# Kernel tuning notes

Hardware: AMD Instinct MI355X
Metric: run time of the kernel (lower is better)

Reference implementation:

```python
import jax, jax.numpy as jnp
import numpy as np

D_MODEL = 768
N_HEADS = 8
HEAD_DIM = D_MODEL // N_HEADS
D_FF = 3072
EPS = 1e-5


def _layernorm(x, g, b):
    mu = jnp.mean(x, axis=-1, keepdims=True)
    var = jnp.var(x, axis=-1, keepdims=True)
    return (x - mu) * jax.lax.rsqrt(var + EPS) * g + b


def setup_inputs() -> dict:
    key = jax.random.key(0)
    ks = jax.random.split(key, 12)
    s = 0.02
    return {
        "x": jax.random.normal(ks[0], (2, 4096, D_MODEL), dtype=jnp.float32),
        "w_qkv": jax.random.normal(ks[1], (D_MODEL, 3 * D_MODEL), dtype=jnp.float32) * s,
        "b_qkv": jnp.zeros((3 * D_MODEL,), dtype=jnp.float32),
        "w_out": jax.random.normal(ks[2], (D_MODEL, D_MODEL), dtype=jnp.float32) * s,
        "b_out": jnp.zeros((D_MODEL,), dtype=jnp.float32),
        "w_ff1": jax.random.normal(ks[3], (D_MODEL, D_FF), dtype=jnp.float32) * s,
        "b_ff1": jnp.zeros((D_FF,), dtype=jnp.float32),
        "w_ff2": jax.random.normal(ks[4], (D_FF, D_MODEL), dtype=jnp.float32) * s,
        "b_ff2": jnp.zeros((D_MODEL,), dtype=jnp.float32),
        "g1": jnp.ones((D_MODEL,), dtype=jnp.float32),
        "be1": jnp.zeros((D_MODEL,), dtype=jnp.float32),
        "g2": jnp.ones((D_MODEL,), dtype=jnp.float32),
        "be2": jnp.zeros((D_MODEL,), dtype=jnp.float32),
    }


def reference(x, w_qkv, b_qkv, w_out, b_out, w_ff1, b_ff1, w_ff2, b_ff2, g1, be1, g2, be2):
    B, S, D = x.shape
    qkv = x @ w_qkv + b_qkv  # [B,S,3D]
    q, k, v = jnp.split(qkv, 3, axis=-1)
    # [B,H,S,d]
    q = q.reshape(B, S, N_HEADS, HEAD_DIM).transpose(0, 2, 1, 3)
    k = k.reshape(B, S, N_HEADS, HEAD_DIM).transpose(0, 2, 1, 3)
    v = v.reshape(B, S, N_HEADS, HEAD_DIM).transpose(0, 2, 1, 3)
    scores = jnp.einsum("bhqd,bhkd->bhqk", q, k) / np.sqrt(HEAD_DIM).astype(np.float32)
    attn = jax.nn.softmax(scores, axis=-1)
    out = jnp.einsum("bhqk,bhkd->bhqd", attn, v)
    out = out.transpose(0, 2, 1, 3).reshape(B, S, D)
    out = out @ w_out + b_out
    x = _layernorm(x + out, g1, be1)
    h = jax.nn.gelu(x @ w_ff1 + b_ff1, approximate=False)
    ffn = h @ w_ff2 + b_ff2
    return _layernorm(x + ffn, g2, be2)
```

## Files before the change

kernel.cpp:

```cpp
#include <hip/hip_runtime.h>
#include <hip/hip_bf16.h>
#include <stdint.h>


typedef __attribute__((ext_vector_type(8))) short bf16x8;
typedef __attribute__((ext_vector_type(4))) short bf16x4;
typedef __attribute__((ext_vector_type(4))) float f32x4;

#define MFMA_BF16(a, b, c) __builtin_amdgcn_mfma_f32_16x16x32_bf16((a), (b), (c), 0, 0, 0)

#define EXP2R(x) __builtin_amdgcn_exp2f(x)

__device__ __forceinline__ short f2bs(float f) {
  return __builtin_bit_cast(short, __float2bfloat16(f));
}
__device__ __forceinline__ float bs2f(short s) {
  union { unsigned u; float f; } v;
  v.u = ((unsigned)(unsigned short)s) << 16;
  return v.f;
}

__device__ __forceinline__ void gload16(const void* g, void* l) {
  __builtin_amdgcn_global_load_lds(
      (const __attribute__((address_space(1))) unsigned int*)g,
      (__attribute__((address_space(3))) unsigned int*)l, 16, 0, 0);
}

__device__ __forceinline__ unsigned ldsoff(const void* p) {
  return (unsigned)(uintptr_t)p;
}

#define TRD(dst, base, off) \
  asm volatile("ds_read_b64_tr_b16 %0, %1 offset:" #off : "=v"(dst) : "v"(base) : "memory")

__global__ __launch_bounds__(256) void transpose_cast(const float* __restrict__ W,
                                                      short* __restrict__ Wt,
                                                      int K, int N) {
  __shared__ float tile[32][33];
  const int n0 = blockIdx.x * 32, k0 = blockIdx.y * 32;
  const int tx = threadIdx.x & 31, ty = threadIdx.x >> 5;
#pragma unroll
  for (int i = 0; i < 4; ++i)
    tile[ty + i * 8][tx] = W[(size_t)(k0 + ty + i * 8) * N + n0 + tx];
  __syncthreads();
#pragma unroll
  for (int i = 0; i < 4; ++i)
    Wt[(size_t)(n0 + ty + i * 8) * K + k0 + tx] = f2bs(tile[tx][ty + i * 8]);
}

__global__ __launch_bounds__(256) void cast_bf16(const float* __restrict__ x,
                                                 short* __restrict__ y, int n4) {
  const int i = blockIdx.x * 256 + threadIdx.x;
  if (i < n4) {
    const float4 v = *(const float4*)(x + (size_t)i * 4);
    short4 o;
    o.x = f2bs(v.x); o.y = f2bs(v.y); o.z = f2bs(v.z); o.w = f2bs(v.w);
    *(short4*)(y + (size_t)i * 4) = o;
  }
}

template <int EPI>
__global__ __launch_bounds__(256) void gemm_bt(const short* __restrict__ A,
                                               const short* __restrict__ Bt,
                                               const float* __restrict__ bias,
                                               void* __restrict__ outp,
                                               int N, int K) {
  __shared__ __align__(16) short ls[3][10240];
  const int tid = threadIdx.x;
  const int lane = tid & 63, w = tid >> 6;
  const int lo = lane & 15, hi = lane >> 4;
  const int wr = w >> 1, wc = w & 1;

  const unsigned gdx = gridDim.x;
  const unsigned nwg = gdx * gridDim.y;
  unsigned lin = blockIdx.y * gdx + blockIdx.x;
  if ((nwg & 7u) == 0u) lin = (lin & 7u) * (nwg >> 3) + (lin >> 3);
  const unsigned by = lin / gdx, bx = lin - by * gdx;
  const int m0 = by * 128, n0 = bx * 128;

  f32x4 acc[4][4] = {};

  const short* rowsrc[5];
#pragma unroll
  for (int s = 0; s < 5; ++s) {
    const int u = s * 256 + tid;
    const int chunk = u / 320;
    const int uin = u - chunk * 320;
    const int r = uin / 5, ui = uin - r * 5;
    const int koff = (ui < 4) ? ui * 8 : 0;
    rowsrc[s] = (chunk < 2 ? A + (size_t)(m0 + chunk * 64 + r) * K
                           : Bt + (size_t)(n0 + (chunk - 2) * 64 + r) * K) + koff;
  }

  auto stage = [&](int kt, int buf) {
    char* base = (char*)ls[buf] + w * 1024;
#pragma unroll
    for (int s = 0; s < 5; ++s)
      gload16(rowsrc[s] + kt, base + s * 4096);
  };

  const int nk = K >> 5;
  stage(0, 0);
  stage(32, 1);
  int cur = 0, nxt = 2;
  for (int t = 0; t < nk; ++t) {
    if (t + 1 < nk) asm volatile("s_waitcnt vmcnt(5)" ::: "memory");
    else            asm volatile("s_waitcnt vmcnt(0)" ::: "memory");
    __builtin_amdgcn_s_barrier();
    asm volatile("" ::: "memory");
    if (t + 2 < nk) stage((t + 2) << 5, nxt);
    bf16x8 af[4], bfr[4];
    const char* lbase = (const char*)ls[cur];
#pragma unroll
    for (int i = 0; i < 4; ++i) {
      af[i]  = *(const bf16x8*)(lbase + (wr * 64 + i * 16 + lo) * 80 + hi * 16);
      bfr[i] = *(const bf16x8*)(lbase + 10240 + (wc * 64 + i * 16 + lo) * 80 + hi * 16);
    }
#pragma unroll
    for (int mi = 0; mi < 4; ++mi)
#pragma unroll
      for (int ni = 0; ni < 4; ++ni)
        acc[mi][ni] = MFMA_BF16(af[mi], bfr[ni], acc[mi][ni]);
    cur = cur == 2 ? 0 : cur + 1;
    nxt = nxt == 2 ? 0 : nxt + 1;
  }

  const int rb = m0 + wr * 64, cb = n0 + wc * 64;
#pragma unroll
  for (int ni = 0; ni < 4; ++ni) {
    const int col = cb + ni * 16 + lo;
    const float bc = bias[col];
#pragma unroll
    for (int mi = 0; mi < 4; ++mi) {
#pragma unroll
      for (int r = 0; r < 4; ++r) {
        const int row = rb + mi * 16 + hi * 4 + r;
        const float v = acc[mi][ni][r] + bc;
        if constexpr (EPI == 0) {
          const int which = col / 768, rem = col - which * 768;
          const int hh = rem / 96, d = rem - hh * 96;
          const int bb = row >> 12, ss = row & 4095;
          ((short*)outp)[((size_t)((which * 2 + bb) * 8 + hh) * 4096 + ss) * 96 + d] = f2bs(v);
        } else if constexpr (EPI == 1) {
          ((short*)outp)[(size_t)row * N + col] = f2bs(v);
        } else {
          const float ge = 0.5f * v * (1.f + erff(v * 0.70710678118654752f));
          ((short*)outp)[(size_t)row * N + col] = f2bs(ge);
        }
      }
    }
  }
}

__global__ __launch_bounds__(256, 3) void attn_fwd(const short* __restrict__ qkv,
                                                   short* __restrict__ out) {
  constexpr int SEQ = 4096;
  constexpr int NT = SEQ / 64;
  constexpr float SCALE2 = 0.10206207261596575f * 1.44269504088896f;
  constexpr float THR2 = 11.5415603f;
  const unsigned linear = blockIdx.x + 32u * (blockIdx.y + 8u * blockIdx.z);
  const int qt = linear >> 4;
  const int hb = linear & 15;
  const int h = hb & 7, b = hb >> 3;
  const int tid = threadIdx.x;
  const int lane = tid & 63, w = tid >> 6;
  const int lo = lane & 15, hi = lane >> 4;

  const size_t headsz = (size_t)SEQ * 96;
  const short* Qh = qkv + (size_t)((0 * 2 + b) * 8 + h) * headsz;
  const short* Kh = qkv + (size_t)((1 * 2 + b) * 8 + h) * headsz;
  const short* Vh = qkv + (size_t)((2 * 2 + b) * 8 + h) * headsz;

  __shared__ __align__(16) short k_lds[6144];
  __shared__ __align__(16) short v_lds[2][6144];
  __shared__ __align__(16) short p_lds[4][2048];

  int voff[3];
#pragma unroll
  for (int t = 0; t < 3; ++t) {
    const int c = t * 256 + tid;
    const int kq = c / 48, rem = c - kq * 48;
    const int dhi = rem >> 3, rem2 = rem & 7;
    voff[t] = (kq * 4 + (rem2 >> 1)) * 96 + dhi * 16 + (rem2 & 1) * 8;
  }

  const int qbase = qt * 128 + w * 32;
  bf16x8 qf[2][3];
#pragma unroll
  for (int f = 0; f < 2; ++f)
#pragma unroll
    for (int dk = 0; dk < 3; ++dk) {
      bf16x8 v = *(const bf16x8*)(Qh + (size_t)(qbase + f * 16 + lo) * 96 + dk * 32 + hi * 8);
#pragma unroll
      for (int i = 0; i < 8; ++i) v[i] = f2bs(bs2f(v[i]) * SCALE2);
      qf[f][dk] = v;
    }

  f32x4 o[2][6] = {};
  float mrow[2][4] = {};
  float lpart[2][4] = {};
  bool escaped = false;

  auto stageK = [&](int t_next) {
    const short* Kt = Kh + (size_t)t_next * 6144;
    char* kd = (char*)k_lds + w * 1024;
#pragma unroll
    for (int t = 0; t < 3; ++t)
      gload16((const char*)Kt + (t * 256 + tid) * 16, kd + t * 4096);
  };
  auto stageV = [&](int t_next, int buf) {
    const short* Vt = Vh + (size_t)t_next * 6144;
    char* vd = (char*)v_lds[buf] + w * 1024;
#pragma unroll
    for (int t = 0; t < 3; ++t)
      gload16(Vt + voff[t], vd + t * 4096);
  };

  stageK(0);
  stageV(0, 0);

  for (int kt = 0; kt < NT; ++kt) {
    const int cur = kt & 1;
    __syncthreads();

    f32x4 s[2][4] = {};
#pragma unroll
    for (int dk = 0; dk < 3; ++dk)
#pragma unroll
      for (int c = 0; c < 4; ++c) {
        const bf16x8 kf = *(const bf16x8*)(k_lds + (c * 16 + lo) * 96 + dk * 32 + hi * 8);
#pragma unroll
        for (int f = 0; f < 2; ++f)
          s[f][c] = MFMA_BF16(qf[f][dk], kf, s[f][c]);
      }

    __syncthreads();
    if (kt + 1 < NT) {
      stageK(kt + 1);
      stageV(kt + 1, cur ^ 1);
    }

    float tm = s[0][0][0];
#pragma unroll
    for (int f = 0; f < 2; ++f)
#pragma unroll
      for (int c = 0; c < 4; ++c)
#pragma unroll
        for (int r = 0; r < 4; ++r) tm = fmaxf(tm, s[f][c][r]);

    if (!__all(tm <= THR2)) {
      escaped = true;
#pragma unroll
      for (int f = 0; f < 2; ++f)
#pragma unroll
        for (int r = 0; r < 4; ++r) {
          float rm = fmaxf(fmaxf(s[f][0][r], s[f][1][r]), fmaxf(s[f][2][r], s[f][3][r]));
          rm = fmaxf(rm, __shfl_xor(rm, 1));
          rm = fmaxf(rm, __shfl_xor(rm, 2));
          rm = fmaxf(rm, __shfl_xor(rm, 4));
          rm = fmaxf(rm, __shfl_xor(rm, 8));
          const float mn = fmaxf(mrow[f][r], rm);
          const float al = EXP2R(mrow[f][r] - mn);
          mrow[f][r] = mn;
          lpart[f][r] *= al;
#pragma unroll
          for (int n = 0; n < 6; ++n) o[f][n][r] *= al;
        }
    }
    if (escaped) {
#pragma unroll
      for (int f = 0; f < 2; ++f)
#pragma unroll
        for (int c = 0; c < 4; ++c)
#pragma unroll
        for (int r = 0; r < 4; ++r) s[f][c][r] = EXP2R(s[f][c][r] - mrow[f][r]);
    } else {
#pragma unroll
      for (int f = 0; f < 2; ++f)
#pragma unroll
        for (int c = 0; c < 4; ++c)
#pragma unroll
        for (int r = 0; r < 4; ++r) s[f][c][r] = EXP2R(s[f][c][r]);
    }

    short* pw = p_lds[w];
#pragma unroll
    for (int f = 0; f < 2; ++f)
#pragma unroll
      for (int c = 0; c < 4; ++c) {
#pragma unroll
        for (int r = 0; r < 4; ++r) lpart[f][r] += s[f][c][r];
        short4 pk;
        pk.x = f2bs(s[f][c][0]);
        pk.y = f2bs(s[f][c][1]);
        pk.z = f2bs(s[f][c][2]);
        pk.w = f2bs(s[f][c][3]);
        *(short4*)(pw + (c * 4 + (lo >> 2)) * 128 + f * 64 + (lo & 3) * 16 + hi * 4) = pk;
      }

    const unsigned vb = ldsoff(v_lds[cur]) + (unsigned)(hi * 1536 + lo * 2);
    const unsigned pb = ldsoff(p_lds[w]) + (unsigned)(hi * 512 + lo * 2);

    {
      bf16x4 va[6], vbh[6], pa0[2], pa1[2];
      TRD(va[0], vb, 0);     TRD(vbh[0], vb, 768);
      TRD(va[1], vb, 128);   TRD(vbh[1], vb, 896);
      TRD(va[2], vb, 256);   TRD(vbh[2], vb, 1024);
      TRD(va[3], vb, 384);   TRD(vbh[3], vb, 1152);
      TRD(va[4], vb, 512);   TRD(vbh[4], vb, 1280);
      TRD(va[5], vb, 640);   TRD(vbh[5], vb, 1408);
      TRD(pa0[0], pb, 0);    TRD(pa1[0], pb, 256);
      TRD(pa0[1], pb, 128);  TRD(pa1[1], pb, 384);
      asm volatile("s_waitcnt lgkmcnt(0)" ::: "memory");
      __builtin_amdgcn_sched_barrier(0);
      __builtin_amdgcn_s_setprio(1);
#pragma unroll
      for (int f = 0; f < 2; ++f) {
        const bf16x8 pf = __builtin_shufflevector(pa0[f], pa1[f], 0, 1, 2, 3, 4, 5, 6, 7);
#pragma unroll
        for (int n = 0; n < 6; ++n) {
          const bf16x8 vf = __builtin_shufflevector(va[n], vbh[n], 0, 1, 2, 3, 4, 5, 6, 7);
          o[f][n] = MFMA_BF16(pf, vf, o[f][n]);
        }
      }
      __builtin_amdgcn_s_setprio(0);
    }
    {
      bf16x4 va[6], vbh[6], pa0[2], pa1[2];
      TRD(va[0], vb, 6144);  TRD(vbh[0], vb, 6912);
      TRD(va[1], vb, 6272);  TRD(vbh[1], vb, 7040);
      TRD(va[2], vb, 6400);  TRD(vbh[2], vb, 7168);
      TRD(va[3], vb, 6528);  TRD(vbh[3], vb, 7296);
      TRD(va[4], vb, 6656);  TRD(vbh[4], vb, 7424);
      TRD(va[5], vb, 6784);  TRD(vbh[5], vb, 7552);
      TRD(pa0[0], pb, 2048); TRD(pa1[0], pb, 2304);
      TRD(pa0[1], pb, 2176); TRD(pa1[1], pb, 2432);
      asm volatile("s_waitcnt lgkmcnt(0)" ::: "memory");
      __builtin_amdgcn_sched_barrier(0);
      __builtin_amdgcn_s_setprio(1);
#pragma unroll
      for (int f = 0; f < 2; ++f) {
        const bf16x8 pf = __builtin_shufflevector(pa0[f], pa1[f], 0, 1, 2, 3, 4, 5, 6, 7);
#pragma unroll
        for (int n = 0; n < 6; ++n) {
          const bf16x8 vf = __builtin_shufflevector(va[n], vbh[n], 0, 1, 2, 3, 4, 5, 6, 7);
          o[f][n] = MFMA_BF16(pf, vf, o[f][n]);
        }
      }
      __builtin_amdgcn_s_setprio(0);
    }
  }

  float inv[2][4];
#pragma unroll
  for (int f = 0; f < 2; ++f)
#pragma unroll
    for (int r = 0; r < 4; ++r) {
      float l = lpart[f][r];
      l += __shfl_xor(l, 1);
      l += __shfl_xor(l, 2);
      l += __shfl_xor(l, 4);
      l += __shfl_xor(l, 8);
      inv[f][r] = 1.f / l;
    }
#pragma unroll
  for (int f = 0; f < 2; ++f)
#pragma unroll
    for (int n = 0; n < 6; ++n)
#pragma unroll
      for (int r = 0; r < 4; ++r) {
        const int q = qbase + f * 16 + hi * 4 + r;
        out[((size_t)(b * SEQ + q)) * 768 + h * 96 + n * 16 + lo] = f2bs(o[f][n][r] * inv[f][r]);
      }
}

template <int MODE>
__global__ __launch_bounds__(192) void ln_residual(const void* __restrict__ xa_,
                                                   const short* __restrict__ xr,
                                                   const float* __restrict__ g,
                                                   const float* __restrict__ be,
                                                   float* __restrict__ outf,
                                                   short* __restrict__ outb) {
  const int row = blockIdx.x, t = threadIdx.x;
  const size_t base = (size_t)row * 768 + t * 4;
  float a0, a1, a2, a3;
  if constexpr (MODE == 0) {
    const float4 a = *(const float4*)((const float*)xa_ + base);
    a0 = a.x; a1 = a.y; a2 = a.z; a3 = a.w;
  } else {
    const short4 a = *(const short4*)((const short*)xa_ + base);
    a0 = bs2f(a.x); a1 = bs2f(a.y); a2 = bs2f(a.z); a3 = bs2f(a.w);
  }
  const short4 bl = *(const short4*)(xr + base);
  const float v0 = a0 + bs2f(bl.x), v1 = a1 + bs2f(bl.y);
  const float v2 = a2 + bs2f(bl.z), v3 = a3 + bs2f(bl.w);
  float s = v0 + v1 + v2 + v3;
  float q = v0 * v0 + v1 * v1 + v2 * v2 + v3 * v3;
#pragma unroll
  for (int m = 32; m; m >>= 1) {
    s += __shfl_xor(s, m);
    q += __shfl_xor(q, m);
  }
  __shared__ float red[2][3];
  const int w = t >> 6;
  if ((t & 63) == 0) { red[0][w] = s; red[1][w] = q; }
  __syncthreads();
  s = red[0][0] + red[0][1] + red[0][2];
  q = red[1][0] + red[1][1] + red[1][2];
  const float mu = s * (1.f / 768.f);
  const float var = q * (1.f / 768.f) - mu * mu;
  const float rstd = rsqrtf(var + 1e-5f);
  const int c = t * 4;
  const float4 gg = *(const float4*)(g + c);
  const float4 bb = *(const float4*)(be + c);
  const float y0 = (v0 - mu) * rstd * gg.x + bb.x;
  const float y1 = (v1 - mu) * rstd * gg.y + bb.y;
  const float y2 = (v2 - mu) * rstd * gg.z + bb.z;
  const float y3 = (v3 - mu) * rstd * gg.w + bb.w;
  if constexpr (MODE == 0) {
    short4 ob;
    ob.x = f2bs(y0); ob.y = f2bs(y1); ob.z = f2bs(y2); ob.w = f2bs(y3);
    *(short4*)(outb + base) = ob;
  } else {
    float4 ov = {y0, y1, y2, y3};
    *(float4*)(outf + base) = ov;
  }
}

extern "C" void kernel_launch(void* const* d_in, const int* in_sizes, int n_in,
                              void* d_out, int out_size, void* d_ws, size_t ws_size,
                              hipStream_t stream) {
  const float* x     = (const float*)d_in[0];
  const float* w_qkv = (const float*)d_in[1];
  const float* b_qkv = (const float*)d_in[2];
  const float* w_out = (const float*)d_in[3];
  const float* b_out = (const float*)d_in[4];
  const float* w_ff1 = (const float*)d_in[5];
  const float* b_ff1 = (const float*)d_in[6];
  const float* w_ff2 = (const float*)d_in[7];
  const float* b_ff2 = (const float*)d_in[8];
  const float* g1  = (const float*)d_in[9];
  const float* be1 = (const float*)d_in[10];
  const float* g2  = (const float*)d_in[11];
  const float* be2 = (const float*)d_in[12];

  char* ws = (char*)d_ws;
  size_t off = 0;
  auto take = [&](size_t bytes) {
    char* p = ws + off;
    off += (bytes + 255) & ~(size_t)255;
    return p;
  };
  short* wqkv_t = (short*)take((size_t)2304 * 768 * 2);
  short* wout_t = (short*)take((size_t)768 * 768 * 2);
  short* wff1_t = (short*)take((size_t)3072 * 768 * 2);
  short* wff2_t = (short*)take((size_t)768 * 3072 * 2);
  short* xb     = (short*)take((size_t)8192 * 768 * 2);
  short* qkv    = (short*)take((size_t)3 * 2 * 8 * 4096 * 96 * 2);
  short* ao     = (short*)take((size_t)8192 * 768 * 2);
  short* x1b    = (short*)take((size_t)8192 * 768 * 2);
  if (ws_size < off) return;

  short* proj = qkv;
  short* hbuf = xb;
  short* ff2o = ao;

  cast_bf16<<<dim3(6144), dim3(256), 0, stream>>>(x, xb, 8192 * 768 / 4);
  transpose_cast<<<dim3(2304 / 32, 768 / 32), dim3(256), 0, stream>>>(w_qkv, wqkv_t, 768, 2304);
  transpose_cast<<<dim3(768 / 32, 768 / 32), dim3(256), 0, stream>>>(w_out, wout_t, 768, 768);
  transpose_cast<<<dim3(3072 / 32, 768 / 32), dim3(256), 0, stream>>>(w_ff1, wff1_t, 768, 3072);
  transpose_cast<<<dim3(768 / 32, 3072 / 32), dim3(256), 0, stream>>>(w_ff2, wff2_t, 3072, 768);

  gemm_bt<0><<<dim3(2304 / 128, 8192 / 128), dim3(256), 0, stream>>>(xb, wqkv_t, b_qkv, qkv, 2304, 768);

  attn_fwd<<<dim3(32, 8, 2), dim3(256), 0, stream>>>(qkv, ao);

  gemm_bt<1><<<dim3(768 / 128, 8192 / 128), dim3(256), 0, stream>>>(ao, wout_t, b_out, proj, 768, 768);

  ln_residual<0><<<dim3(8192), dim3(192), 0, stream>>>(x, proj, g1, be1, nullptr, x1b);

  gemm_bt<2><<<dim3(3072 / 128, 8192 / 128), dim3(256), 0, stream>>>(x1b, wff1_t, b_ff1, hbuf, 3072, 768);

  gemm_bt<1><<<dim3(768 / 128, 8192 / 128), dim3(256), 0, stream>>>(hbuf, wff2_t, b_ff2, ff2o, 768, 3072);

  ln_residual<1><<<dim3(8192), dim3(192), 0, stream>>>(x1b, ff2o, g2, be2, (float*)d_out, nullptr);
}
```

Measured before the change: 357.9 us.

## Split attention KV range into two halves and merge partial outputs

Attention is split along the key dimension: each query tile is handled by two blocks covering half the keys each, doubling the grid from 512 to 1024 blocks. Each block writes an unnormalized bf16 partial output plus per-row max and sum, and a new merge kernel combines the two with log-sum-exp rescaling before the output projection. This targets low occupancy or poor wave balance on a many-CU GPU. In exchange it adds extra global traffic, one more kernel launch, and rounding of unnormalized partials to bf16.

```diff
diff --git a/kernel.cpp b/kernel.cpp
--- a/kernel.cpp
+++ b/kernel.cpp
@@ -153,15 +153,18 @@
 }
 
 __global__ __launch_bounds__(256, 3) void attn_fwd(const short* __restrict__ qkv,
-                                                   short* __restrict__ out) {
+                                                   short* __restrict__ op0,
+                                                   short* __restrict__ op1,
+                                                   float2* __restrict__ ml) {
   constexpr int SEQ = 4096;
-  constexpr int NT = SEQ / 64;
   constexpr float SCALE2 = 0.10206207261596575f * 1.44269504088896f;
   constexpr float THR2 = 11.5415603f;
-  const unsigned linear = blockIdx.x + 32u * (blockIdx.y + 8u * blockIdx.z);
-  const int qt = linear >> 4;
+  const unsigned linear = blockIdx.x + 64u * (blockIdx.y + 8u * blockIdx.z);
+  const int qt2 = linear >> 4;
+  const int qt = qt2 >> 1, half = qt2 & 1;
   const int hb = linear & 15;
   const int h = hb & 7, b = hb >> 3;
+  const int kt0 = half * 32, kt1 = kt0 + 32;
   const int tid = threadIdx.x;
   const int lane = tid & 63, w = tid >> 6;
   const int lo = lane & 15, hi = lane >> 4;
@@ -170,6 +173,7 @@
   const short* Qh = qkv + (size_t)((0 * 2 + b) * 8 + h) * headsz;
   const short* Kh = qkv + (size_t)((1 * 2 + b) * 8 + h) * headsz;
   const short* Vh = qkv + (size_t)((2 * 2 + b) * 8 + h) * headsz;
+  short* Op = half ? op1 : op0;
 
   __shared__ __align__(16) short k_lds[6144];
   __shared__ __align__(16) short v_lds[2][6144];
@@ -216,10 +220,10 @@
       gload16(Vt + voff[t], vd + t * 4096);
   };
 
-  stageK(0);
-  stageV(0, 0);
-
-  for (int kt = 0; kt < NT; ++kt) {
+  stageK(kt0);
+  stageV(kt0, 0);
+
+  for (int kt = kt0; kt < kt1; ++kt) {
     const int cur = kt & 1;
     __syncthreads();
 
@@ -235,7 +239,7 @@
       }
 
     __syncthreads();
-    if (kt + 1 < NT) {
+    if (kt + 1 < kt1) {
       stageK(kt + 1);
       stageV(kt + 1, cur ^ 1);
     }
@@ -351,7 +355,7 @@
     }
   }
 
-  float inv[2][4];
+  float lred[2][4];
 #pragma unroll
   for (int f = 0; f < 2; ++f)
 #pragma unroll
@@ -361,7 +365,7 @@
       l += __shfl_xor(l, 2);
       l += __shfl_xor(l, 4);
       l += __shfl_xor(l, 8);
-      inv[f][r] = 1.f / l;
+      lred[f][r] = l;
     }
 #pragma unroll
   for (int f = 0; f < 2; ++f)
@@ -370,8 +374,42 @@
 #pragma unroll
       for (int r = 0; r < 4; ++r) {
         const int q = qbase + f * 16 + hi * 4 + r;
-        out[((size_t)(b * SEQ + q)) * 768 + h * 96 + n * 16 + lo] = f2bs(o[f][n][r] * inv[f][r]);
-      }
+        Op[((size_t)(b * SEQ + q)) * 768 + h * 96 + n * 16 + lo] = f2bs(o[f][n][r]);
+      }
+  if (lo == 0) {
+#pragma unroll
+    for (int f = 0; f < 2; ++f)
+#pragma unroll
+      for (int r = 0; r < 4; ++r) {
+        const int q = qbase + f * 16 + hi * 4 + r;
+        ml[(size_t)((half * 2 + b) * 8 + h) * SEQ + q] = make_float2(mrow[f][r], lred[f][r]);
+      }
+  }
+}
+
+__global__ __launch_bounds__(192) void attn_merge(const short* __restrict__ op0,
+                                                  const short* __restrict__ op1,
+                                                  const float2* __restrict__ ml,
+                                                  short* __restrict__ out) {
+  const int row = blockIdx.x;
+  const int b = row >> 12, q = row & 4095;
+  const int t = threadIdx.x;
+  const int col = t * 4;
+  const int h = col / 96;
+  const float2 m0 = ml[(size_t)((0 * 2 + b) * 8 + h) * 4096 + q];
+  const float2 m1 = ml[(size_t)((1 * 2 + b) * 8 + h) * 4096 + q];
+  const float m = fmaxf(m0.x, m1.x);
+  const float a0 = EXP2R(m0.x - m), a1 = EXP2R(m1.x - m);
+  const float inv = 1.f / (a0 * m0.y + a1 * m1.y);
+  const size_t base = (size_t)row * 768 + col;
+  const short4 v0 = *(const short4*)(op0 + base);
+  const short4 v1 = *(const short4*)(op1 + base);
+  short4 ov;
+  ov.x = f2bs((bs2f(v0.x) * a0 + bs2f(v1.x) * a1) * inv);
+  ov.y = f2bs((bs2f(v0.y) * a0 + bs2f(v1.y) * a1) * inv);
+  ov.z = f2bs((bs2f(v0.z) * a0 + bs2f(v1.z) * a1) * inv);
+  ov.w = f2bs((bs2f(v0.w) * a0 + bs2f(v1.w) * a1) * inv);
+  *(short4*)(out + base) = ov;
 }
 
 template <int MODE>
@@ -459,8 +497,12 @@
   short* qkv    = (short*)take((size_t)3 * 2 * 8 * 4096 * 96 * 2);
   short* ao     = (short*)take((size_t)8192 * 768 * 2);
   short* x1b    = (short*)take((size_t)8192 * 768 * 2);
+  short* mrg    = (short*)take((size_t)8192 * 768 * 2);
+  float2* ml    = (float2*)take((size_t)32 * 4096 * 8);
   if (ws_size < off) return;
 
+  short* op0  = xb;
+  short* op1  = ao;
   short* proj = qkv;
   short* hbuf = xb;
   short* ff2o = ao;
@@ -473,9 +515,10 @@
 
   gemm_bt<0><<<dim3(2304 / 128, 8192 / 128), dim3(256), 0, stream>>>(xb, wqkv_t, b_qkv, qkv, 2304, 768);
 
-  attn_fwd<<<dim3(32, 8, 2), dim3(256), 0, stream>>>(qkv, ao);
-
-  gemm_bt<1><<<dim3(768 / 128, 8192 / 128), dim3(256), 0, stream>>>(ao, wout_t, b_out, proj, 768, 768);
+  attn_fwd<<<dim3(64, 8, 2), dim3(256), 0, stream>>>(qkv, op0, op1, ml);
+  attn_merge<<<dim3(8192), dim3(192), 0, stream>>>(op0, op1, ml, mrg);
+
+  gemm_bt<1><<<dim3(768 / 128, 8192 / 128), dim3(256), 0, stream>>>(mrg, wout_t, b_out, proj, 768, 768);
 
   ln_residual<0><<<dim3(8192), dim3(192), 0, stream>>>(x, proj, g1, be1, nullptr, x1b);
 
```

After: 371.5 us. +3.8%, slower.
